# Kernel optimization log

Measured on AMD Instinct MI355X. Metric: run time of the kernel, lower is better.

The kernel has to match this reference:

```python
import jax, jax.numpy as jnp
import numpy as np

TEMPERATURE = 0.2
EPS = 1e-12  # matches torch F.normalize eps


def _l2_normalize(x):
    n = jnp.linalg.norm(x, axis=-1, keepdims=True)
    return x / jnp.maximum(n, EPS)


def setup_inputs() -> dict:
    key = jax.random.key(0)
    k1, k2 = jax.random.split(key)
    B, D = 8192, 256
    return {
        "user_embeddings": jax.random.normal(k1, (B, D), dtype=jnp.float32),
        "positive_item_embeddings": jax.random.normal(k2, (B, D), dtype=jnp.float32),
    }


def reference(user_embeddings, positive_item_embeddings):
    # all_item_embeddings=None branch: in-batch implicit negatives.
    u = _l2_normalize(user_embeddings)            # [B, D]
    p = _l2_normalize(positive_item_embeddings)   # [B, D]
    sim = jnp.einsum("bd,nd->bn", u, p) / TEMPERATURE  # [B, B]
    pos_sim = jnp.diagonal(sim)                   # [B]; equals the torch pos_sim
    # Original concatenates pos_sim[i] with the off-diagonal row entries and takes
    # logsumexp. Since the diagonal of sim IS pos_sim[i], that set equals the full
    # row, so loss_i = -pos_sim_i + logsumexp(sim[i, :]). Vectorized over the batch.
    lse = jax.nn.logsumexp(sim, axis=1)           # [B]
    return jnp.mean(lse - pos_sim)
```

## Files before the change

kernel.cpp:

```cpp
#include <hip/hip_runtime.h>
#include <hip/hip_bf16.h>

#define DDIM 256
#define NROWS 8192

typedef __attribute__((ext_vector_type(8))) __bf16 bf16x8;
typedef __attribute__((ext_vector_type(4))) float floatx4;

__device__ __forceinline__ void async16(const void* g, void* l) {
    __builtin_amdgcn_global_load_lds(
        (const __attribute__((address_space(1))) unsigned int*)g,
        (__attribute__((address_space(3))) unsigned int*)l,
        16, 0, 0);
}

__global__ __launch_bounds__(256) void normalize_kernel(
    const float* __restrict__ U, const float* __restrict__ P,
    unsigned short* __restrict__ Un, unsigned short* __restrict__ Pn,
    float* __restrict__ possim, float* __restrict__ rowsum)
{
    const int lane = threadIdx.x & 63;
    const int row  = blockIdx.x * 4 + (threadIdx.x >> 6);
    const size_t base = (size_t)row * DDIM + lane * 4;
    const float4 u4 = *(const float4*)(U + base);
    const float4 p4 = *(const float4*)(P + base);
    float su = u4.x*u4.x + u4.y*u4.y + u4.z*u4.z + u4.w*u4.w;
    float sp = p4.x*p4.x + p4.y*p4.y + p4.z*p4.z + p4.w*p4.w;
    float up = u4.x*p4.x + u4.y*p4.y + u4.z*p4.z + u4.w*p4.w;
    #pragma unroll
    for (int d = 1; d < 64; d <<= 1) {
        su += __shfl_xor(su, d);
        sp += __shfl_xor(sp, d);
        up += __shfl_xor(up, d);
    }
    const float iu = rsqrtf(fmaxf(su, 1e-24f));
    const float ip = rsqrtf(fmaxf(sp, 1e-24f));
    if (lane == 0) {
        possim[row] = up * iu * ip;
        rowsum[row] = 0.0f;
    }
    union { ushort4 s4; __hip_bfloat16 h[4]; } cu, cp;
    cu.h[0] = __float2bfloat16(u4.x * iu); cu.h[1] = __float2bfloat16(u4.y * iu);
    cu.h[2] = __float2bfloat16(u4.z * iu); cu.h[3] = __float2bfloat16(u4.w * iu);
    cp.h[0] = __float2bfloat16(p4.x * ip); cp.h[1] = __float2bfloat16(p4.y * ip);
    cp.h[2] = __float2bfloat16(p4.z * ip); cp.h[3] = __float2bfloat16(p4.w * ip);
    *(ushort4*)(Un + base) = cu.s4;
    *(ushort4*)(Pn + base) = cp.s4;
}

__global__ __launch_bounds__(256, 3) void sim_exp_rowsum(
    const unsigned short* __restrict__ Un,
    const unsigned short* __restrict__ Pn,
    float* __restrict__ rowsum)
{
    __shared__ __align__(16) unsigned short As[128 * 64];
    __shared__ __align__(16) unsigned short Bs[128 * 64];
    const int tid  = threadIdx.x;
    const int lane = tid & 63;
    const int wv   = tid >> 6;
    const int wr   = wv >> 1, wc = wv & 1;
    const int rowblock = blockIdx.y, colblock = blockIdx.x;

    floatx4 acc[4][4];
    #pragma unroll
    for (int t = 0; t < 4; ++t)
        #pragma unroll
        for (int u = 0; u < 4; ++u)
            acc[t][u] = {0.0f, 0.0f, 0.0f, 0.0f};

    const int srow = lane >> 3;
    const int gg   = (lane & 7) ^ srow;
    const size_t abase = (size_t)rowblock * 128 * DDIM;
    const size_t bbase = (size_t)colblock * 128 * DDIM;
    const int q = lane >> 4;
    const int m = lane & 15;

    #pragma unroll
    for (int kc = 0; kc < 4; ++kc) {
        const int k0 = kc * 64;
        __syncthreads();
        #pragma unroll
        for (int i = 0; i < 4; ++i) {
            const int rg = wv * 4 + i;
            const int r  = rg * 8 + srow;
            async16(Un + abase + (size_t)r * DDIM + k0 + gg * 8, &As[rg * 8 * 64]);
            async16(Pn + bbase + (size_t)r * DDIM + k0 + gg * 8, &Bs[rg * 8 * 64]);
        }
        __syncthreads();
        #pragma unroll
        for (int ks = 0; ks < 2; ++ks) {
            bf16x8 af[4], bfr[4];
            const int gl = ks * 4 + q;
            const int gp = (gl ^ (m & 7)) * 8;
            #pragma unroll
            for (int t = 0; t < 4; ++t) {
                af[t]  = *(const bf16x8*)&As[(wr * 64 + t * 16 + m) * 64 + gp];
                bfr[t] = *(const bf16x8*)&Bs[(wc * 64 + t * 16 + m) * 64 + gp];
            }
            #pragma unroll
            for (int t = 0; t < 4; ++t)
                #pragma unroll
                for (int u = 0; u < 4; ++u)
                    acc[t][u] = __builtin_amdgcn_mfma_f32_16x16x32_bf16(
                        af[t], bfr[u], acc[t][u], 0, 0, 0);
        }
    }

    #pragma unroll
    for (int t = 0; t < 4; ++t) {
        #pragma unroll
        for (int r = 0; r < 4; ++r) {
            float s = __expf(5.0f * acc[t][0][r]) + __expf(5.0f * acc[t][1][r])
                    + __expf(5.0f * acc[t][2][r]) + __expf(5.0f * acc[t][3][r]);
            s += __shfl_xor(s, 1);
            s += __shfl_xor(s, 2);
            s += __shfl_xor(s, 4);
            s += __shfl_xor(s, 8);
            if (m == 0) {
                const int grow = rowblock * 128 + wr * 64 + t * 16 + q * 4 + r;
                atomicAdd(&rowsum[grow], s);
            }
        }
    }
}

__global__ __launch_bounds__(256) void finalize_kernel(
    const float* __restrict__ rowsum, const float* __restrict__ possim,
    float* __restrict__ out)
{
    float acc = 0.0f;
    for (int i = threadIdx.x; i < NROWS; i += 256)
        acc += __logf(rowsum[i]) - 5.0f * possim[i];
    #pragma unroll
    for (int d = 1; d < 64; d <<= 1) acc += __shfl_xor(acc, d);
    __shared__ float wsum[4];
    if ((threadIdx.x & 63) == 0) wsum[threadIdx.x >> 6] = acc;
    __syncthreads();
    if (threadIdx.x == 0)
        out[0] = (wsum[0] + wsum[1] + wsum[2] + wsum[3]) * (1.0f / (float)NROWS);
}

extern "C" void kernel_launch(void* const* d_in, const int* in_sizes, int n_in,
                              void* d_out, int out_size, void* d_ws, size_t ws_size,
                              hipStream_t stream) {
    const float* U = (const float*)d_in[0];
    const float* P = (const float*)d_in[1];
    float* out = (float*)d_out;
    char* ws = (char*)d_ws;
    unsigned short* Un = (unsigned short*)ws;
    unsigned short* Pn = (unsigned short*)(ws + 4194304);
    float* rowsum = (float*)(ws + 8388608);
    float* possim = (float*)(ws + 8388608 + 32768);

    normalize_kernel<<<NROWS / 4, 256, 0, stream>>>(U, P, Un, Pn, possim, rowsum);
    dim3 g2(64, 64);
    sim_exp_rowsum<<<g2, 256, 0, stream>>>(Un, Pn, rowsum);
    finalize_kernel<<<1, 256, 0, stream>>>(rowsum, possim, out);
}
```

Measured before the change: 158.3 us.

## Keep A stripe in registers, stream double-buffered B tiles, fuse finalize

Each block now owns a 128-row stripe of normalized users, holds the full K=256 A fragments in registers, and streams 1024 positive rows in 64-row double-buffered LDS tiles. Exponentials are accumulated per row across tiles, which cuts the atomics to one set per block. The grid shrinks from 4096 to 512 blocks, and the finalize kernel is folded into the last block through a ticket counter. The goal is to remove redundant A reloads, per-tile atomics and one kernel launch. The cost is high register pressure (launch bounds dropped to 2 waves) and fewer blocks to spread across the CUs.

```diff
diff --git a/kernel.cpp b/kernel.cpp
--- a/kernel.cpp
+++ b/kernel.cpp
@@ -14,11 +14,36 @@
         16, 0, 0);
 }
 
+__device__ __forceinline__ void stage_rows(const unsigned short* __restrict__ g,
+                                           unsigned short* l,
+                                           int wv, int lane,
+                                           int rows_per_wave, int ninstr)
+{
+    const int lrow = lane >> 5;
+    const int gcol = lane & 31;
+    const int r0 = wv * rows_per_wave;
+    for (int j = 0; j < ninstr; ++j) {
+        const int rb = r0 + j * 2;
+        const int r  = rb + lrow;
+        const int gg = gcol ^ (r & 7);
+        async16(g + (size_t)r * DDIM + gg * 8, l + (size_t)rb * DDIM);
+    }
+}
+
+__device__ __forceinline__ bf16x8 frag(const unsigned short* base, int row,
+                                       int ks, int q, int m)
+{
+    return *(const bf16x8*)&base[(size_t)row * DDIM
+                                 + (((ks * 4 + q) ^ (m & 7)) * 8)];
+}
+
 __global__ __launch_bounds__(256) void normalize_kernel(
     const float* __restrict__ U, const float* __restrict__ P,
     unsigned short* __restrict__ Un, unsigned short* __restrict__ Pn,
-    float* __restrict__ possim, float* __restrict__ rowsum)
-{
+    float* __restrict__ possim, float* __restrict__ rowsum,
+    float* __restrict__ out, int* __restrict__ counter)
+{
+    if (blockIdx.x == 0 && threadIdx.x == 0) { out[0] = 0.0f; counter[0] = 0; }
     const int lane = threadIdx.x & 63;
     const int row  = blockIdx.x * 4 + (threadIdx.x >> 6);
     const size_t base = (size_t)row * DDIM + lane * 4;
@@ -48,96 +73,119 @@
     *(ushort4*)(Pn + base) = cp.s4;
 }
 
-__global__ __launch_bounds__(256, 3) void sim_exp_rowsum(
+__global__ __launch_bounds__(256, 2) void sim_exp_rowsum(
     const unsigned short* __restrict__ Un,
     const unsigned short* __restrict__ Pn,
-    float* __restrict__ rowsum)
-{
-    __shared__ __align__(16) unsigned short As[128 * 64];
-    __shared__ __align__(16) unsigned short Bs[128 * 64];
+    float* __restrict__ rowsum,
+    const float* __restrict__ possim,
+    int* __restrict__ counter,
+    float* __restrict__ out)
+{
+    __shared__ __align__(16) unsigned short lds[32768];
+    __shared__ float ws4[4];
+    __shared__ int ticket_s;
+
     const int tid  = threadIdx.x;
     const int lane = tid & 63;
     const int wv   = tid >> 6;
     const int wr   = wv >> 1, wc = wv & 1;
-    const int rowblock = blockIdx.y, colblock = blockIdx.x;
-
-    floatx4 acc[4][4];
+    const int m = lane & 15;
+    const int q = lane >> 4;
+
+    const int stripe = blockIdx.x >> 3;
+    const int oct    = blockIdx.x & 7;
+
+    const unsigned short* Aglob = Un + (size_t)stripe * 128 * DDIM;
+    stage_rows(Aglob, lds, wv, lane, 32, 16);
+    __syncthreads();
+
+    bf16x8 afr[4][8];
     #pragma unroll
     for (int t = 0; t < 4; ++t)
         #pragma unroll
-        for (int u = 0; u < 4; ++u)
-            acc[t][u] = {0.0f, 0.0f, 0.0f, 0.0f};
-
-    const int srow = lane >> 3;
-    const int gg   = (lane & 7) ^ srow;
-    const size_t abase = (size_t)rowblock * 128 * DDIM;
-    const size_t bbase = (size_t)colblock * 128 * DDIM;
-    const int q = lane >> 4;
-    const int m = lane & 15;
-
-    #pragma unroll
-    for (int kc = 0; kc < 4; ++kc) {
-        const int k0 = kc * 64;
+        for (int ks = 0; ks < 8; ++ks)
+            afr[t][ks] = frag(lds, wr * 64 + t * 16 + m, ks, q, m);
+    __syncthreads();
+
+    const unsigned short* Bglob = Pn + (size_t)(oct * 1024) * DDIM;
+    float rowpart[4][4];
+    #pragma unroll
+    for (int t = 0; t < 4; ++t)
+        #pragma unroll
+        for (int r = 0; r < 4; ++r)
+            rowpart[t][r] = 0.0f;
+
+    stage_rows(Bglob, lds, wv, lane, 16, 8);
+
+    for (int i = 0; i < 16; ++i) {
         __syncthreads();
-        #pragma unroll
-        for (int i = 0; i < 4; ++i) {
-            const int rg = wv * 4 + i;
-            const int r  = rg * 8 + srow;
-            async16(Un + abase + (size_t)r * DDIM + k0 + gg * 8, &As[rg * 8 * 64]);
-            async16(Pn + bbase + (size_t)r * DDIM + k0 + gg * 8, &Bs[rg * 8 * 64]);
-        }
-        __syncthreads();
-        #pragma unroll
-        for (int ks = 0; ks < 2; ++ks) {
-            bf16x8 af[4], bfr[4];
-            const int gl = ks * 4 + q;
-            const int gp = (gl ^ (m & 7)) * 8;
+        if (i < 15)
+            stage_rows(Bglob + (size_t)(i + 1) * 64 * DDIM,
+                       lds + ((i + 1) & 1) * 16384, wv, lane, 16, 8);
+        const unsigned short* Bp = lds + (i & 1) * 16384;
+
+        floatx4 acc[4][2];
+        #pragma unroll
+        for (int t = 0; t < 4; ++t) {
+            acc[t][0] = {0.0f, 0.0f, 0.0f, 0.0f};
+            acc[t][1] = {0.0f, 0.0f, 0.0f, 0.0f};
+        }
+        #pragma unroll
+        for (int ks = 0; ks < 8; ++ks) {
+            const bf16x8 b0 = frag(Bp, wc * 32 + m,      ks, q, m);
+            const bf16x8 b1 = frag(Bp, wc * 32 + 16 + m, ks, q, m);
             #pragma unroll
             for (int t = 0; t < 4; ++t) {
-                af[t]  = *(const bf16x8*)&As[(wr * 64 + t * 16 + m) * 64 + gp];
-                bfr[t] = *(const bf16x8*)&Bs[(wc * 64 + t * 16 + m) * 64 + gp];
+                acc[t][0] = __builtin_amdgcn_mfma_f32_16x16x32_bf16(
+                    afr[t][ks], b0, acc[t][0], 0, 0, 0);
+                acc[t][1] = __builtin_amdgcn_mfma_f32_16x16x32_bf16(
+                    afr[t][ks], b1, acc[t][1], 0, 0, 0);
             }
+        }
+        #pragma unroll
+        for (int t = 0; t < 4; ++t)
             #pragma unroll
-            for (int t = 0; t < 4; ++t)
-                #pragma unroll
-                for (int u = 0; u < 4; ++u)
-                    acc[t][u] = __builtin_amdgcn_mfma_f32_16x16x32_bf16(
-                        af[t], bfr[u], acc[t][u], 0, 0, 0);
-        }
+            for (int r = 0; r < 4; ++r)
+                rowpart[t][r] += __expf(5.0f * acc[t][0][r])
+                               + __expf(5.0f * acc[t][1][r]);
     }
 
     #pragma unroll
     for (int t = 0; t < 4; ++t) {
         #pragma unroll
         for (int r = 0; r < 4; ++r) {
-            float s = __expf(5.0f * acc[t][0][r]) + __expf(5.0f * acc[t][1][r])
-                    + __expf(5.0f * acc[t][2][r]) + __expf(5.0f * acc[t][3][r]);
+            float s = rowpart[t][r];
             s += __shfl_xor(s, 1);
             s += __shfl_xor(s, 2);
             s += __shfl_xor(s, 4);
             s += __shfl_xor(s, 8);
             if (m == 0) {
-                const int grow = rowblock * 128 + wr * 64 + t * 16 + q * 4 + r;
+                const int grow = stripe * 128 + wr * 64 + t * 16 + q * 4 + r;
                 atomicAdd(&rowsum[grow], s);
             }
         }
     }
-}
-
-__global__ __launch_bounds__(256) void finalize_kernel(
-    const float* __restrict__ rowsum, const float* __restrict__ possim,
-    float* __restrict__ out)
-{
-    float acc = 0.0f;
-    for (int i = threadIdx.x; i < NROWS; i += 256)
-        acc += __logf(rowsum[i]) - 5.0f * possim[i];
-    #pragma unroll
-    for (int d = 1; d < 64; d <<= 1) acc += __shfl_xor(acc, d);
-    __shared__ float wsum[4];
-    if ((threadIdx.x & 63) == 0) wsum[threadIdx.x >> 6] = acc;
-    __syncthreads();
-    if (threadIdx.x == 0)
-        out[0] = (wsum[0] + wsum[1] + wsum[2] + wsum[3]) * (1.0f / (float)NROWS);
+
+    __threadfence();
+    __syncthreads();
+    if (tid == 0)
+        ticket_s = __hip_atomic_fetch_add(counter, 1, __ATOMIC_ACQ_REL,
+                                          __HIP_MEMORY_SCOPE_AGENT);
+    __syncthreads();
+    if (ticket_s == 511) {
+        float part = 0.0f;
+        for (int i = tid; i < NROWS; i += 256) {
+            const float rs = __hip_atomic_load(&rowsum[i], __ATOMIC_RELAXED,
+                                               __HIP_MEMORY_SCOPE_AGENT);
+            part += __logf(rs) - 5.0f * possim[i];
+        }
+        #pragma unroll
+        for (int d = 1; d < 64; d <<= 1) part += __shfl_xor(part, d);
+        if (lane == 0) ws4[wv] = part;
+        __syncthreads();
+        if (tid == 0)
+            out[0] = (ws4[0] + ws4[1] + ws4[2] + ws4[3]) * (1.0f / (float)NROWS);
+    }
 }
 
 extern "C" void kernel_launch(void* const* d_in, const int* in_sizes, int n_in,
@@ -151,9 +199,9 @@
     unsigned short* Pn = (unsigned short*)(ws + 4194304);
     float* rowsum = (float*)(ws + 8388608);
     float* possim = (float*)(ws + 8388608 + 32768);
-
-    normalize_kernel<<<NROWS / 4, 256, 0, stream>>>(U, P, Un, Pn, possim, rowsum);
-    dim3 g2(64, 64);
-    sim_exp_rowsum<<<g2, 256, 0, stream>>>(Un, Pn, rowsum);
-    finalize_kernel<<<1, 256, 0, stream>>>(rowsum, possim, out);
-}
+    int* counter  = (int*)(ws + 8388608 + 65536);
+
+    normalize_kernel<<<NROWS / 4, 256, 0, stream>>>(U, P, Un, Pn, possim, rowsum,
+                                                    out, counter);
+    sim_exp_rowsum<<<512, 256, 0, stream>>>(Un, Pn, rowsum, possim, counter, out);
+}
```

New measurement: 144.6 us. -8.6%, faster.
